# Performance work log

Hardware: AMD Instinct MI355X
Metric: run time of the kernel (lower is better)

Reference implementation:

```python
import jax, jax.numpy as jnp
import numpy as np

B, S, HID = 2, 2048, 2048
H, KH, D = 16, 4, 128  # heads, kv heads, head_dim
N_REP = H // KH
SCALE = D ** -0.5


def rotate_half(x):
    x1, x2 = x[..., : D // 2], x[..., D // 2:]
    return jnp.concatenate((-x2, x1), axis=-1)


def setup_inputs() -> dict:
    key = jax.random.key(0)
    ks = jax.random.split(key, 6)
    hidden_states = jax.random.normal(ks[0], (B, S, HID), jnp.float32)
    # standard RoPE cos/sin tables, shape [B, S, D]
    inv_freq = 1.0 / (10000.0 ** (np.arange(0, D, 2, dtype=np.float32) / D))
    pos = np.arange(S, dtype=np.float32)
    freqs = np.outer(pos, inv_freq)            # [S, D/2]
    emb = np.concatenate([freqs, freqs], -1)   # [S, D]
    cos = jnp.broadcast_to(jnp.cos(emb), (B, S, D)).astype(jnp.float32)
    sin = jnp.broadcast_to(jnp.sin(emb), (B, S, D)).astype(jnp.float32)
    # additive causal mask [1, 1, S, S]
    neg = jnp.finfo(jnp.float32).min
    causal = jnp.triu(jnp.full((S, S), neg, jnp.float32), k=1)
    attention_mask = causal[None, None]
    std = 0.02
    wq = jax.random.normal(ks[1], (HID, H * D), jnp.float32) * std
    wk = jax.random.normal(ks[2], (HID, KH * D), jnp.float32) * std
    wv = jax.random.normal(ks[3], (HID, KH * D), jnp.float32) * std
    wo = jax.random.normal(ks[4], (H * D, HID), jnp.float32) * std
    return {"hidden_states": hidden_states, "cos": cos, "sin": sin,
            "attention_mask": attention_mask, "wq": wq, "wk": wk, "wv": wv, "wo": wo}


def reference(hidden_states, cos, sin, attention_mask, wq, wk, wv, wo):
    b, s, _ = hidden_states.shape
    q = (hidden_states @ wq).reshape(b, s, H, D).transpose(0, 2, 1, 3)   # [b,H,s,d]
    k = (hidden_states @ wk).reshape(b, s, KH, D).transpose(0, 2, 1, 3)  # [b,KH,s,d]
    v = (hidden_states @ wv).reshape(b, s, KH, D).transpose(0, 2, 1, 3)
    c = cos[:, None, :, :]  # [b,1,s,d] broadcast over heads
    sn = sin[:, None, :, :]
    q = q * c + rotate_half(q) * sn
    k = k * c + rotate_half(k) * sn
    # GQA: repeat KV heads
    k = jnp.repeat(k, N_REP, axis=1)  # [b,H,s,d]
    v = jnp.repeat(v, N_REP, axis=1)
    scores = jnp.einsum('bhqd,bhkd->bhqk', q, k) * SCALE + attention_mask
    probs = jax.nn.softmax(scores, axis=-1)
    attn = jnp.einsum('bhqk,bhkd->bhqd', probs, v)
    attn = attn.transpose(0, 2, 1, 3).reshape(b, s, H * D)
    return attn @ wo
```

## Files before the change

kernel.cpp:

```cpp
#include <hip/hip_runtime.h>
#include <stdint.h>

#define Bc   2
#define Sc   2048
#define HIDc 2048
#define Hc   16
#define KHc  4
#define Dc   128
#define HDc  2048
#define KHDc 512
#define QKVS 3072
#define SCALEc 0.08838834764831845f
#define N_ITEMS 1024

typedef _Float16 f16;
typedef _Float16 f16x2 __attribute__((ext_vector_type(2)));
typedef _Float16 f16x4 __attribute__((ext_vector_type(4)));
typedef _Float16 f16x8 __attribute__((ext_vector_type(8)));
typedef float    f32x4 __attribute__((ext_vector_type(4)));

__device__ __forceinline__ void gl_lds16(const void* g, void* l) {
  __builtin_amdgcn_global_load_lds(
      (const __attribute__((address_space(1))) unsigned int*)g,
      (__attribute__((address_space(3))) unsigned int*)l, 16, 0, 0);
}

__global__ __launch_bounds__(256) void conv_hs(const float* __restrict__ in,
                                               f16* __restrict__ out,
                                               int* __restrict__ ctr) {
  if (blockIdx.x == 0 && threadIdx.x == 0) *ctr = 0;
  int i = (blockIdx.x * 256 + threadIdx.x) * 4;
  float4 v = *(const float4*)&in[i];
  f16x4 o; o[0] = (f16)v.x; o[1] = (f16)v.y; o[2] = (f16)v.z; o[3] = (f16)v.w;
  *(f16x4*)&out[i] = o;
}

__global__ __launch_bounds__(256) void trw_all(const float* __restrict__ wq,
                                               const float* __restrict__ wk,
                                               const float* __restrict__ wv,
                                               const float* __restrict__ wo,
                                               f16* __restrict__ wqkvT,
                                               f16* __restrict__ woT) {
  const int z = blockIdx.z;
  const float* in; f16* out; int C, rowOff;
  if (z == 0)      { in = wq; out = wqkvT; C = 2048; rowOff = 0; }
  else if (z == 1) { in = wk; out = wqkvT; C = 512;  rowOff = 2048; }
  else if (z == 2) { in = wv; out = wqkvT; C = 512;  rowOff = 2560; }
  else             { in = wo; out = woT;   C = 2048; rowOff = 0; }
  if (blockIdx.x * 64 >= C) return;
  __shared__ float Ld[64 * 65];
  const int tid = threadIdx.x;
  const int r0 = blockIdx.y * 64, c0 = blockIdx.x * 64;
#pragma unroll
  for (int p = 0; p < 4; ++p) {
    int idx = p * 256 + tid;
    int r = idx >> 4, c4 = (idx & 15) * 4;
    float4 v = *(const float4*)&in[(size_t)(r0 + r) * C + c0 + c4];
    Ld[r * 65 + c4 + 0] = v.x; Ld[r * 65 + c4 + 1] = v.y;
    Ld[r * 65 + c4 + 2] = v.z; Ld[r * 65 + c4 + 3] = v.w;
  }
  __syncthreads();
#pragma unroll
  for (int p = 0; p < 4; ++p) {
    int idx = p * 256 + tid;
    int oc = idx >> 4, m4 = (idx & 15) * 4;
    f16x4 o;
#pragma unroll
    for (int i = 0; i < 4; ++i) o[i] = (f16)Ld[(m4 + i) * 65 + oc];
    *(f16x4*)&out[(size_t)(rowOff + c0 + oc) * 2048 + r0 + m4] = o;
  }
}

__global__ __launch_bounds__(256) void rope_all(f16* __restrict__ x,
                                                const float* __restrict__ cb,
                                                const float* __restrict__ sb) {
  int bid = blockIdx.x;
  int colbase, log2h, idx;
  if (bid < 16384) { colbase = 0;    log2h = 4; idx = bid * 256 + threadIdx.x; }
  else             { colbase = 2048; log2h = 2; idx = (bid - 16384) * 256 + threadIdx.x; }
  int d   = idx & 63;
  int h   = (idx >> 6) & ((1 << log2h) - 1);
  int row = idx >> (6 + log2h);
  f16* p = x + (size_t)row * QKVS + colbase + h * 128;
  float x1 = (float)p[d], x2 = (float)p[64 + d];
  float c = cb[(size_t)row * 128 + d], s = sb[(size_t)row * 128 + d];
  p[d]      = (f16)(x1 * c - x2 * s);
  p[64 + d] = (f16)(x2 * c + x1 * s);
}

__global__ __launch_bounds__(256) void v_tr(const f16* __restrict__ QKV,
                                            f16* __restrict__ Vt) {
  __shared__ f16 Ld[64 * 78];
  const int tid = threadIdx.x;
  const int s0 = blockIdx.x * 64, d0 = blockIdx.y * 64;
  const int b = blockIdx.z >> 2, kh = blockIdx.z & 3;
#pragma unroll
  for (int p = 0; p < 2; ++p) {
    int idx = p * 256 + tid;
    int sl = idx >> 3, dc8 = (idx & 7) * 8;
    f16x8 v = *(const f16x8*)&QKV[(size_t)(b * Sc + s0 + sl) * QKVS + 2560 + kh * 128 + d0 + dc8];
#pragma unroll
    for (int i = 0; i < 4; ++i) {
      f16x2 w; w[0] = v[2 * i]; w[1] = v[2 * i + 1];
      *(f16x2*)&Ld[sl * 78 + dc8 + 2 * i] = w;
    }
  }
  __syncthreads();
  {
    int dr = (tid >> 3) * 2, sc8 = (tid & 7) * 8;
    f16x8 r0v, r1v;
#pragma unroll
    for (int j = 0; j < 8; ++j) {
      f16x2 w = *(const f16x2*)&Ld[(sc8 + j) * 78 + dr];
      r0v[j] = w[0]; r1v[j] = w[1];
    }
    size_t obase = ((size_t)(b * KHc + kh) * 128 + d0 + dr) * Sc + s0 + sc8;
    *(f16x8*)&Vt[obase]      = r0v;
    *(f16x8*)&Vt[obase + Sc] = r1v;
  }
}

__global__ __launch_bounds__(256) void gemm_bt(const f16* __restrict__ A,
                                               const f16* __restrict__ Bt,
                                               void* __restrict__ Cout,
                                               int M, int N, int K, int c_f16) {
  __shared__ f16 Al[128 * 64];
  __shared__ f16 Bl[128 * 64];
  const int tid  = threadIdx.x;
  const int lane = tid & 63, wave = tid >> 6;
  const int quad = lane >> 4, l16 = lane & 15;
  const int wm = (wave >> 1) * 64, wn = (wave & 1) * 64;
  const int m0 = blockIdx.y * 128, n0 = blockIdx.x * 128;
  f32x4 acc[4][4] = {};

  for (int k0 = 0; k0 < K; k0 += 64) {
    __syncthreads();
#pragma unroll
    for (int p = 0; p < 4; ++p) {
      const int g  = wave * 2 + (p >> 1);
      const int kq = (p & 1) * 4 + quad;
      gl_lds16(&A [(size_t)(m0 + g * 16 + l16) * K + k0 + kq * 8], &Al[(wave * 4 + p) * 64 * 8]);
      gl_lds16(&Bt[(size_t)(n0 + g * 16 + l16) * K + k0 + kq * 8], &Bl[(wave * 4 + p) * 64 * 8]);
    }
    __syncthreads();
#pragma unroll
    for (int ks = 0; ks < 2; ++ks) {
      f16x8 af[4], bf[4];
#pragma unroll
      for (int i = 0; i < 4; ++i)
        af[i] = *(const f16x8*)&Al[((((wave >> 1) * 4 + i) * 8 + ks * 4 + quad) * 16 + l16) * 8];
#pragma unroll
      for (int j = 0; j < 4; ++j)
        bf[j] = *(const f16x8*)&Bl[((((wave & 1) * 4 + j) * 8 + ks * 4 + quad) * 16 + l16) * 8];
#pragma unroll
      for (int i = 0; i < 4; ++i)
#pragma unroll
        for (int j = 0; j < 4; ++j)
          acc[i][j] = __builtin_amdgcn_mfma_f32_16x16x32_f16(af[i], bf[j], acc[i][j], 0, 0, 0);
    }
  }

  if (c_f16) {
    f16* C = (f16*)Cout;
#pragma unroll
    for (int i = 0; i < 4; ++i)
#pragma unroll
      for (int j = 0; j < 4; ++j)
#pragma unroll
        for (int r = 0; r < 4; ++r)
          C[(size_t)(m0 + wm + i * 16 + quad * 4 + r) * N + n0 + wn + j * 16 + l16] =
              (f16)acc[i][j][r];
  } else {
    float* C = (float*)Cout;
#pragma unroll
    for (int i = 0; i < 4; ++i)
#pragma unroll
      for (int j = 0; j < 4; ++j)
#pragma unroll
        for (int r = 0; r < 4; ++r)
          C[(size_t)(m0 + wm + i * 16 + quad * 4 + r) * N + n0 + wn + j * 16 + l16] =
              acc[i][j][r];
  }
}

__global__ __launch_bounds__(256, 4) void attn_v3(const f16* __restrict__ QKV,
                                                  const f16* __restrict__ Vt,
                                                  f16* __restrict__ Ob,
                                                  int* __restrict__ ctr) {
  __shared__ f16 Kl[64 * 128];
  __shared__ f16 Vl[64 * 128];
  __shared__ f16 Ps[4 * 512];
  __shared__ int item_s;
  const int tid  = threadIdx.x;
  const int lane = tid & 63, wave = tid >> 6;
  const int quad = lane >> 4, l16 = lane & 15;

  for (;;) {
    if (tid == 0) item_s = atomicAdd(ctr, 1);
    __syncthreads();
    const int item = item_s;
    if (item >= N_ITEMS) break;
    const int qt = 31 - (item >> 5);
    const int bh = item & 31;
    const int b = bh >> 4, h = bh & 15, kh = h >> 2;
    const int qbase = qt * 64 + wave * 16;

    f16x8 qf[4];
    {
      const f16* qp = QKV + (size_t)(b * Sc + qbase + l16) * QKVS + h * 128 + quad * 8;
#pragma unroll
      for (int c = 0; c < 4; ++c) qf[c] = *(const f16x8*)(qp + c * 32);
    }
    float m_i[4] = {-1e30f, -1e30f, -1e30f, -1e30f};
    float l_i[4] = {0.f, 0.f, 0.f, 0.f};
    f32x4 o[8] = {};

    const int ktiles = qt + 1;
    for (int kt = 0; kt < ktiles; ++kt) {
      __syncthreads();
#pragma unroll
      for (int p = 0; p < 4; ++p) {
        gl_lds16(&QKV[(size_t)(b * Sc + kt * 64 + wave * 16 + l16) * QKVS + 2048 + kh * 128 + p * 32 + quad * 8],
                 &Kl[(wave * 4 + p) * 512]);
        const int dt = wave * 2 + (p >> 1), kc = p & 1;
        gl_lds16(&Vt[(size_t)((b * KHc + kh) * 128 + dt * 16 + l16) * Sc + kt * 64 + kc * 32 + quad * 8],
                 &Vl[(wave * 4 + p) * 512]);
      }
      __syncthreads();

      f32x4 s[4] = {};
#pragma unroll
      for (int kc = 0; kc < 2; ++kc)
#pragma unroll
        for (int c = 0; c < 4; ++c) {
          f16x8 ka = *(const f16x8*)&Kl[(((kc * 2 + 0) * 4 + c) * 4 + quad) * 128 + l16 * 8];
          f16x8 kb = *(const f16x8*)&Kl[(((kc * 2 + 1) * 4 + c) * 4 + quad) * 128 + l16 * 8];
          s[kc * 2 + 0] = __builtin_amdgcn_mfma_f32_16x16x32_f16(qf[c], ka, s[kc * 2 + 0], 0, 0, 0);
          s[kc * 2 + 1] = __builtin_amdgcn_mfma_f32_16x16x32_f16(qf[c], kb, s[kc * 2 + 1], 0, 0, 0);
        }

      const int cb = kt * 64 + l16;
      const int wb = wave * 512 + (l16 & 7);
      const int rhi = l16 >> 3;
      float e2[4], e3[4], alpha[4];
#pragma unroll
      for (int r = 0; r < 4; ++r) {
        int qrow = qbase + quad * 4 + r;
        float v0 = s[0][r] * SCALEc, v1 = s[1][r] * SCALEc;
        float v2 = s[2][r] * SCALEc, v3 = s[3][r] * SCALEc;
        if (cb      > qrow) v0 = -1e30f;
        if (cb + 16 > qrow) v1 = -1e30f;
        if (cb + 32 > qrow) v2 = -1e30f;
        if (cb + 48 > qrow) v3 = -1e30f;
        float mx = fmaxf(fmaxf(v0, v1), fmaxf(v2, v3));
        mx = fmaxf(mx, __shfl_xor(mx, 1));
        mx = fmaxf(mx, __shfl_xor(mx, 2));
        mx = fmaxf(mx, __shfl_xor(mx, 4));
        mx = fmaxf(mx, __shfl_xor(mx, 8));
        float mnew = fmaxf(m_i[r], mx);
        float al = __expf(m_i[r] - mnew);
        v0 = __expf(v0 - mnew); v1 = __expf(v1 - mnew);
        v2 = __expf(v2 - mnew); v3 = __expf(v3 - mnew);
        float rs = (v0 + v1) + (v2 + v3);
        rs += __shfl_xor(rs, 1);
        rs += __shfl_xor(rs, 2);
        rs += __shfl_xor(rs, 4);
        rs += __shfl_xor(rs, 8);
        l_i[r] = l_i[r] * al + rs;
        m_i[r] = mnew;
        alpha[r] = al;
        int rowoff = (quad * 4 + r) * 8;
        Ps[wb + (rhi + 0) * 128 + rowoff] = (f16)v0;
        Ps[wb + (rhi + 2) * 128 + rowoff] = (f16)v1;
        e2[r] = v2; e3[r] = v3;
      }
#pragma unroll
      for (int dt = 0; dt < 8; ++dt)
#pragma unroll
        for (int r = 0; r < 4; ++r) o[dt][r] *= alpha[r];

      {
        f16x8 pf = *(const f16x8*)&Ps[wave * 512 + quad * 128 + l16 * 8];
#pragma unroll
        for (int dt = 0; dt < 8; ++dt) {
          f16x8 vf = *(const f16x8*)&Vl[((dt * 2 + 0) * 4 + quad) * 128 + l16 * 8];
          o[dt] = __builtin_amdgcn_mfma_f32_16x16x32_f16(pf, vf, o[dt], 0, 0, 0);
        }
      }
#pragma unroll
      for (int r = 0; r < 4; ++r) {
        int rowoff = (quad * 4 + r) * 8;
        Ps[wb + (rhi + 0) * 128 + rowoff] = (f16)e2[r];
        Ps[wb + (rhi + 2) * 128 + rowoff] = (f16)e3[r];
      }
      {
        f16x8 pf = *(const f16x8*)&Ps[wave * 512 + quad * 128 + l16 * 8];
#pragma unroll
        for (int dt = 0; dt < 8; ++dt) {
          f16x8 vf = *(const f16x8*)&Vl[((dt * 2 + 1) * 4 + quad) * 128 + l16 * 8];
          o[dt] = __builtin_amdgcn_mfma_f32_16x16x32_f16(pf, vf, o[dt], 0, 0, 0);
        }
      }
    }

    float inv[4];
#pragma unroll
    for (int r = 0; r < 4; ++r) inv[r] = 1.0f / l_i[r];
#pragma unroll
    for (int dt = 0; dt < 8; ++dt)
#pragma unroll
      for (int r = 0; r < 4; ++r)
        Ob[(size_t)(b * Sc + qbase + quad * 4 + r) * HDc + h * 128 + dt * 16 + l16] =
            (f16)(o[dt][r] * inv[r]);
  }
}

extern "C" void kernel_launch(void* const* d_in, const int* in_sizes, int n_in,
                              void* d_out, int out_size, void* d_ws, size_t ws_size,
                              hipStream_t stream) {
  (void)in_sizes; (void)n_in; (void)out_size; (void)ws_size;
  const float* hs   = (const float*)d_in[0];
  const float* cosb = (const float*)d_in[1];
  const float* sinb = (const float*)d_in[2];
  const float* wq = (const float*)d_in[4];
  const float* wk = (const float*)d_in[5];
  const float* wv = (const float*)d_in[6];
  const float* wo = (const float*)d_in[7];
  float* out = (float*)d_out;

  char* ws = (char*)d_ws;
  int*  ctr = (int*)ws;
  size_t off = 256;
  auto alloc = [&](size_t elems) { f16* p = (f16*)(ws + off); off += elems * sizeof(f16); return p; };
  f16* hsF    = alloc((size_t)Bc * Sc * HIDc);
  f16* wqkvT  = alloc((size_t)QKVS * HIDc);
  f16* woT    = alloc((size_t)HIDc * HDc);
  f16* QKVf   = alloc((size_t)Bc * Sc * QKVS);
  f16* Vt_g   = alloc((size_t)Bc * KHc * Dc * Sc);
  f16* attnF  = hsF;

  conv_hs<<<8192, 256, 0, stream>>>(hs, hsF, ctr);
  trw_all<<<dim3(32, 32, 4), 256, 0, stream>>>(wq, wk, wv, wo, wqkvT, woT);

  gemm_bt<<<dim3(24, 32), 256, 0, stream>>>(hsF, wqkvT, QKVf, 4096, QKVS, 2048, 1);

  rope_all<<<20480, 256, 0, stream>>>(QKVf, cosb, sinb);
  v_tr<<<dim3(32, 2, 8), 256, 0, stream>>>(QKVf, Vt_g);

  attn_v3<<<1024, 256, 0, stream>>>(QKVf, Vt_g, attnF, ctr);

  gemm_bt<<<dim3(16, 32), 256, 0, stream>>>(attnF, woT, out, 4096, 2048, 2048, 0);
}
```

Baseline: 466.8 us.

## Split long causal attention tiles across KV halves and merge partial results

Query tiles 16-31 are split into two work items, each covering half the KV range. Each half writes a normalized partial output plus its row max and sum, and a new merge kernel combines them, so the persistent scheduler gets more even work items. The softmax now uses exp2 with the scale folded in by log2(e), and the row sum is taken with an MFMA against a ones vector instead of cross-lane shuffles. The cost is an extra kernel launch, extra global traffic for the partials, and workspace reuse of the wqkvT buffer for them.

Result: faster. 450.3 us (-3.5%).

```diff
diff --git a/kernel.cpp b/kernel.cpp
--- a/kernel.cpp
+++ b/kernel.cpp
@@ -10,8 +10,8 @@
 #define HDc  2048
 #define KHDc 512
 #define QKVS 3072
-#define SCALEc 0.08838834764831845f
-#define N_ITEMS 1024
+#define SCALE2c 0.12751744657f
+#define N_ITEMS 1536
 
 typedef _Float16 f16;
 typedef _Float16 f16x2 __attribute__((ext_vector_type(2)));
@@ -139,8 +139,8 @@
     for (int p = 0; p < 4; ++p) {
       const int g  = wave * 2 + (p >> 1);
       const int kq = (p & 1) * 4 + quad;
-      gl_lds16(&A [(size_t)(m0 + g * 16 + l16) * K + k0 + kq * 8], &Al[(wave * 4 + p) * 64 * 8]);
-      gl_lds16(&Bt[(size_t)(n0 + g * 16 + l16) * K + k0 + kq * 8], &Bl[(wave * 4 + p) * 64 * 8]);
+      gl_lds16(&A [(size_t)(m0 + g * 16 + l16) * K + k0 + kq * 8], &Al[(wave * 4 + p) * 512]);
+      gl_lds16(&Bt[(size_t)(n0 + g * 16 + l16) * K + k0 + kq * 8], &Bl[(wave * 4 + p) * 512]);
     }
     __syncthreads();
 #pragma unroll
@@ -183,9 +183,11 @@
   }
 }
 
-__global__ __launch_bounds__(256, 4) void attn_v3(const f16* __restrict__ QKV,
+__global__ __launch_bounds__(256, 4) void attn_v4(const f16* __restrict__ QKV,
                                                   const f16* __restrict__ Vt,
                                                   f16* __restrict__ Ob,
+                                                  f16* __restrict__ Opart,
+                                                  float2* __restrict__ ML,
                                                   int* __restrict__ ctr) {
   __shared__ f16 Kl[64 * 128];
   __shared__ f16 Vl[64 * 128];
@@ -195,13 +197,37 @@
   const int lane = tid & 63, wave = tid >> 6;
   const int quad = lane >> 4, l16 = lane & 15;
 
+  f16x8 ones_f;
+#pragma unroll
+  for (int i = 0; i < 8; ++i) ones_f[i] = (l16 == 0) ? (f16)1.0f : (f16)0.0f;
+
   for (;;) {
     if (tid == 0) item_s = atomicAdd(ctr, 1);
     __syncthreads();
     const int item = item_s;
     if (item >= N_ITEMS) break;
-    const int qt = 31 - (item >> 5);
-    const int bh = item & 31;
+
+    int qt, bh, k0t, k1t, hf = -1;
+    if (item < 1280) {
+      int base = 0, c = 32;
+#pragma unroll 1
+      for (; c >= 17; --c) {
+        int sz = (c & 1) ? 64 : 96;
+        if (item < base + sz) break;
+        base += sz;
+      }
+      int off = item - base;
+      if (off < 64) {
+        qt = c - 1; hf = off >> 5; bh = off & 31;
+        int nk = qt + 1, hn = nk >> 1;
+        k0t = hf ? hn : 0; k1t = hf ? nk : hn;
+      } else {
+        qt = (c >> 1) - 1; bh = off - 64; k0t = 0; k1t = qt + 1;
+      }
+    } else {
+      int off = item - 1280;
+      qt = 7 - (off >> 5); bh = off & 31; k0t = 0; k1t = qt + 1;
+    }
     const int b = bh >> 4, h = bh & 15, kh = h >> 2;
     const int qbase = qt * 64 + wave * 16;
 
@@ -212,11 +238,10 @@
       for (int c = 0; c < 4; ++c) qf[c] = *(const f16x8*)(qp + c * 32);
     }
     float m_i[4] = {-1e30f, -1e30f, -1e30f, -1e30f};
-    float l_i[4] = {0.f, 0.f, 0.f, 0.f};
+    f32x4 ls = {};
     f32x4 o[8] = {};
 
-    const int ktiles = qt + 1;
-    for (int kt = 0; kt < ktiles; ++kt) {
+    for (int kt = k0t; kt < k1t; ++kt) {
       __syncthreads();
 #pragma unroll
       for (int p = 0; p < 4; ++p) {
@@ -246,8 +271,8 @@
 #pragma unroll
       for (int r = 0; r < 4; ++r) {
         int qrow = qbase + quad * 4 + r;
-        float v0 = s[0][r] * SCALEc, v1 = s[1][r] * SCALEc;
-        float v2 = s[2][r] * SCALEc, v3 = s[3][r] * SCALEc;
+        float v0 = s[0][r] * SCALE2c, v1 = s[1][r] * SCALE2c;
+        float v2 = s[2][r] * SCALE2c, v3 = s[3][r] * SCALE2c;
         if (cb      > qrow) v0 = -1e30f;
         if (cb + 16 > qrow) v1 = -1e30f;
         if (cb + 32 > qrow) v2 = -1e30f;
@@ -258,29 +283,25 @@
         mx = fmaxf(mx, __shfl_xor(mx, 4));
         mx = fmaxf(mx, __shfl_xor(mx, 8));
         float mnew = fmaxf(m_i[r], mx);
-        float al = __expf(m_i[r] - mnew);
-        v0 = __expf(v0 - mnew); v1 = __expf(v1 - mnew);
-        v2 = __expf(v2 - mnew); v3 = __expf(v3 - mnew);
-        float rs = (v0 + v1) + (v2 + v3);
-        rs += __shfl_xor(rs, 1);
-        rs += __shfl_xor(rs, 2);
-        rs += __shfl_xor(rs, 4);
-        rs += __shfl_xor(rs, 8);
-        l_i[r] = l_i[r] * al + rs;
+        alpha[r] = exp2f(m_i[r] - mnew);
         m_i[r] = mnew;
-        alpha[r] = al;
+        v0 = exp2f(v0 - mnew); v1 = exp2f(v1 - mnew);
+        v2 = exp2f(v2 - mnew); v3 = exp2f(v3 - mnew);
         int rowoff = (quad * 4 + r) * 8;
         Ps[wb + (rhi + 0) * 128 + rowoff] = (f16)v0;
         Ps[wb + (rhi + 2) * 128 + rowoff] = (f16)v1;
         e2[r] = v2; e3[r] = v3;
       }
 #pragma unroll
+      for (int r = 0; r < 4; ++r) ls[r] *= alpha[r];
+#pragma unroll
       for (int dt = 0; dt < 8; ++dt)
 #pragma unroll
         for (int r = 0; r < 4; ++r) o[dt][r] *= alpha[r];
 
       {
         f16x8 pf = *(const f16x8*)&Ps[wave * 512 + quad * 128 + l16 * 8];
+        ls = __builtin_amdgcn_mfma_f32_16x16x32_f16(pf, ones_f, ls, 0, 0, 0);
 #pragma unroll
         for (int dt = 0; dt < 8; ++dt) {
           f16x8 vf = *(const f16x8*)&Vl[((dt * 2 + 0) * 4 + quad) * 128 + l16 * 8];
@@ -295,6 +316,7 @@
       }
       {
         f16x8 pf = *(const f16x8*)&Ps[wave * 512 + quad * 128 + l16 * 8];
+        ls = __builtin_amdgcn_mfma_f32_16x16x32_f16(pf, ones_f, ls, 0, 0, 0);
 #pragma unroll
         for (int dt = 0; dt < 8; ++dt) {
           f16x8 vf = *(const f16x8*)&Vl[((dt * 2 + 1) * 4 + quad) * 128 + l16 * 8];
@@ -303,15 +325,64 @@
       }
     }
 
-    float inv[4];
-#pragma unroll
-    for (int r = 0; r < 4; ++r) inv[r] = 1.0f / l_i[r];
-#pragma unroll
-    for (int dt = 0; dt < 8; ++dt)
-#pragma unroll
-      for (int r = 0; r < 4; ++r)
-        Ob[(size_t)(b * Sc + qbase + quad * 4 + r) * HDc + h * 128 + dt * 16 + l16] =
-            (f16)(o[dt][r] * inv[r]);
+    float inv[4], lrow[4];
+#pragma unroll
+    for (int r = 0; r < 4; ++r) {
+      lrow[r] = __shfl(ls[r], lane & 48);
+      inv[r] = 1.0f / lrow[r];
+    }
+    if (hf < 0) {
+#pragma unroll
+      for (int dt = 0; dt < 8; ++dt)
+#pragma unroll
+        for (int r = 0; r < 4; ++r)
+          Ob[(size_t)(b * Sc + qbase + quad * 4 + r) * HDc + h * 128 + dt * 16 + l16] =
+              (f16)(o[dt][r] * inv[r]);
+    } else {
+      const int tile = (qt - 16) * 32 + bh;
+      f16* op = Opart + ((size_t)tile * 2 + hf) * (64 * 128);
+#pragma unroll
+      for (int dt = 0; dt < 8; ++dt)
+#pragma unroll
+        for (int r = 0; r < 4; ++r)
+          op[(wave * 16 + quad * 4 + r) * 128 + dt * 16 + l16] = (f16)(o[dt][r] * inv[r]);
+      if (l16 == 0) {
+#pragma unroll
+        for (int r = 0; r < 4; ++r) {
+          float2 ml; ml.x = m_i[r]; ml.y = lrow[r];
+          ML[((size_t)tile * 2 + hf) * 64 + wave * 16 + quad * 4 + r] = ml;
+        }
+      }
+    }
+  }
+}
+
+__global__ __launch_bounds__(256) void attn_merge(const f16* __restrict__ Opart,
+                                                  const float2* __restrict__ ML,
+                                                  f16* __restrict__ Ob) {
+  const int tile = blockIdx.x;
+  const int qt = 16 + (tile >> 5), bh = tile & 31;
+  const int b = bh >> 4, h = bh & 15;
+  const int tid = threadIdx.x;
+  const int row = tid >> 2, c0 = (tid & 3) * 32;
+  float2 ml1 = ML[(size_t)tile * 2 * 64 + row];
+  float2 ml2 = ML[((size_t)tile * 2 + 1) * 64 + row];
+  float m = fmaxf(ml1.x, ml2.x);
+  float w1 = ml1.y * exp2f(ml1.x - m);
+  float w2 = ml2.y * exp2f(ml2.x - m);
+  float rinv = 1.0f / (w1 + w2);
+  float a1 = w1 * rinv, a2 = w2 * rinv;
+  const f16* o1 = Opart + (size_t)tile * 2 * (64 * 128) + row * 128 + c0;
+  const f16* o2 = o1 + 64 * 128;
+  f16* out = Ob + (size_t)(b * Sc + qt * 64 + row) * HDc + h * 128 + c0;
+#pragma unroll
+  for (int j = 0; j < 4; ++j) {
+    f16x8 x1 = *(const f16x8*)(o1 + j * 8);
+    f16x8 x2 = *(const f16x8*)(o2 + j * 8);
+    f16x8 y;
+#pragma unroll
+    for (int i = 0; i < 8; ++i) y[i] = (f16)(a1 * (float)x1[i] + a2 * (float)x2[i]);
+    *(f16x8*)(out + j * 8) = y;
   }
 }
 
@@ -331,13 +402,18 @@
   char* ws = (char*)d_ws;
   int*  ctr = (int*)ws;
   size_t off = 256;
-  auto alloc = [&](size_t elems) { f16* p = (f16*)(ws + off); off += elems * sizeof(f16); return p; };
-  f16* hsF    = alloc((size_t)Bc * Sc * HIDc);
-  f16* wqkvT  = alloc((size_t)QKVS * HIDc);
-  f16* woT    = alloc((size_t)HIDc * HDc);
-  f16* QKVf   = alloc((size_t)Bc * Sc * QKVS);
-  f16* Vt_g   = alloc((size_t)Bc * KHc * Dc * Sc);
-  f16* attnF  = hsF;
+  auto alloc = [&](size_t bytes) { char* p = ws + off; off += (bytes + 255) & ~(size_t)255; return p; };
+  f16*  hsF   = (f16*)alloc((size_t)Bc * Sc * HIDc * 2);
+  f16*  woT   = (f16*)alloc((size_t)HIDc * HDc * 2);
+  f16*  QKVf  = (f16*)alloc((size_t)Bc * Sc * QKVS * 2);
+  f16*  Vt_g  = (f16*)alloc((size_t)Bc * KHc * Dc * Sc * 2);
+  f16*  wqkvT = (f16*)alloc((size_t)QKVS * HIDc * 2);
+  f16*  Opart = wqkvT;
+  size_t opart_bytes = (size_t)512 * 2 * 64 * 128 * 2;
+  size_t wqkvT_bytes = (size_t)QKVS * HIDc * 2;
+  if (opart_bytes > wqkvT_bytes) off += opart_bytes - wqkvT_bytes;
+  float2* ML = (float2*)alloc((size_t)512 * 2 * 64 * sizeof(float2));
+  f16*  attnF = hsF;
 
   conv_hs<<<8192, 256, 0, stream>>>(hs, hsF, ctr);
   trw_all<<<dim3(32, 32, 4), 256, 0, stream>>>(wq, wk, wv, wo, wqkvT, woT);
@@ -347,7 +423,8 @@
   rope_all<<<20480, 256, 0, stream>>>(QKVf, cosb, sinb);
   v_tr<<<dim3(32, 2, 8), 256, 0, stream>>>(QKVf, Vt_g);
 
-  attn_v3<<<1024, 256, 0, stream>>>(QKVf, Vt_g, attnF, ctr);
+  attn_v4<<<1024, 256, 0, stream>>>(QKVf, Vt_g, attnF, Opart, ML, ctr);
+  attn_merge<<<512, 256, 0, stream>>>(Opart, ML, attnF);
 
   gemm_bt<<<dim3(16, 32), 256, 0, stream>>>(attnF, woT, out, 4096, 2048, 2048, 0);
 }
```
